# Kernel tuning notes

Hardware: AMD Instinct MI355X
Metric: run time of the kernel (lower is better)

Reference implementation:

```python
import jax, jax.numpy as jnp
import numpy as np

EPS = 1e-5
B, T, D = 4, 2048, 512
H, DK, DV = 4, 64, 128  # num_heads, head_qk_dim, head_v_dim
LR = 32                 # proj_low_rank_dim


def ln(x, g, b):
    m = jnp.mean(x, -1, keepdims=True)
    v = jnp.var(x, -1, keepdims=True)
    return (x - m) * jax.lax.rsqrt(v + EPS) * g + b


def shift(x):  # token shift: zero-pad one step in time
    return jnp.pad(x, ((0, 0), (1, 0), (0, 0)))[:, :-1]


def setup_inputs() -> dict:
    key = jax.random.key(0)
    ks = iter(jax.random.split(key, 40))
    rn = lambda shape, s=0.02: jax.random.normal(next(ks), shape, jnp.float32) * s
    return dict(
        x=jax.random.normal(next(ks), (B, T, D), jnp.float32),
        ln0_g=jnp.ones((D,), jnp.float32), ln0_b=jnp.zeros((D,), jnp.float32),
        ln1_g=jnp.ones((D,), jnp.float32), ln1_b=jnp.zeros((D,), jnp.float32),
        ln2_g=jnp.ones((D,), jnp.float32), ln2_b=jnp.zeros((D,), jnp.float32),
        xp_mu=jax.random.uniform(next(ks), (D,), jnp.float32),
        xp_w1=rn((5 * LR, D)),
        xp_w2=rn((D, 5 * LR)),
        x_bias=rn((5, D)),
        r_w=rn((H * DK, D)),
        w_A=rn((64, D)), w_B=rn((H * DK, 64)), w_b=rn((H * DK,)),
        k_w=rn((H * DK, D)),
        v_w=rn((H * DV, D)),
        g_w=rn((H * DV, D)),
        bonus=rn((H, DK)),
        gn_g=jnp.ones((DV,), jnp.float32), gn_b=jnp.zeros((DV,), jnp.float32),
        o_w=rn((D, H * DV)),
        fk_mu=jax.random.uniform(next(ks), (D,), jnp.float32),
        fk_w=rn((1024, D)),
        fr_mu=jax.random.uniform(next(ks), (D,), jnp.float32),
        fr_w=rn((D, D)),
        fv_w=rn((D, 1024)),
    )


def reference(x, ln0_g, ln0_b, ln1_g, ln1_b, ln2_g, ln2_b, xp_mu, xp_w1, xp_w2,
              x_bias, r_w, w_A, w_B, w_b, k_w, v_w, g_w, bonus, gn_g, gn_b,
              o_w, fk_mu, fk_w, fr_mu, fr_w, fv_w):
    # --- block pre-norm (layer_idx==0) and attn norm ---
    residual = ln(x, ln0_g, ln0_b)
    h = ln(residual, ln1_g, ln1_b)

    # --- RWKV6 time mixing ---
    delta = shift(h) - h
    xx = jnp.tanh(((h + delta * xp_mu) @ xp_w1.T).reshape(B, T, 5, LR))
    mods = jnp.einsum('btnr,hnr->btnh', xx, xp_w2.reshape(D, 5, LR)) + x_bias
    mr, mw, mk, mv, mg = (mods[:, :, i] for i in range(5))

    r = ((h + delta * mr) @ r_w.T).reshape(B, T, H, DK)
    wl = jnp.tanh((h + delta * mw) @ w_A.T) @ w_B.T + w_b  # LoRA decay proj
    dec = jnp.exp(-jnp.exp(wl)).reshape(B, T, H, DK)       # per-channel decay in (0,1)
    k = ((h + delta * mk) @ k_w.T).reshape(B, T, H, DK)
    v = ((h + delta * mv) @ v_w.T).reshape(B, T, H, DV)
    g = (h + delta * mg) @ g_w.T

    def step(S, inp):
        r_t, k_t, v_t, d_t = inp                           # (B,H,DK),(B,H,DK),(B,H,DV),(B,H,DK)
        kv = k_t[..., :, None] * v_t[..., None, :]          # (B,H,DK,DV)
        o_t = jnp.einsum('bhk,bhkv->bhv', r_t, S + bonus[None, :, :, None] * kv)
        S = d_t[..., None] * S + kv
        return S, o_t

    tf = lambda a: jnp.moveaxis(a, 1, 0)  # time-major for scan
    S0 = jnp.zeros((B, H, DK, DV), x.dtype)
    _, o = jax.lax.scan(step, S0, (tf(r), tf(k), tf(v), tf(dec)))
    o = jnp.moveaxis(o, 0, 1)  # (B,T,H,DV)

    # fused per-head LayerNorm + swish gate, then output proj
    gg = g.reshape(B, T, H, DV)
    o = ln(o, gn_g, gn_b) * (gg * jax.nn.sigmoid(gg))
    a = o.reshape(B, T, H * DV) @ o_w.T

    # --- channel mixing FFN with residual ---
    z = a + residual
    h2 = ln(z, ln2_g, ln2_b)
    d2 = shift(h2) - h2
    kk = jnp.square(jax.nn.relu((h2 + d2 * fk_mu) @ fk_w.T))
    rr = jax.nn.sigmoid((h2 + d2 * fr_mu) @ fr_w.T)
    return z + rr * (kk @ fv_w.T)
```

## Files before the change

### kernel.cpp

```cpp
#include <hip/hip_runtime.h>
#include <math.h>

constexpr int Bq = 4, Tq = 2048, Dq = 512, Hq = 4, DKq = 64, DVq = 128, LRq = 32;
constexpr int Mq = Bq * Tq;
constexpr float EPSq = 1e-5f;
constexpr int CL2 = 32, NC2 = Tq / CL2, BH2 = Bq * Hq;

typedef unsigned short u16;
typedef __attribute__((ext_vector_type(8))) short short8v;
typedef __attribute__((ext_vector_type(4))) float f32x4;

__device__ __forceinline__ u16 f2b(float f) {
    unsigned u = __float_as_uint(f);
    u += 0x7fffu + ((u >> 16) & 1);
    return (u16)(u >> 16);
}

__device__ __forceinline__ void gl_lds16(const void* g, void* l) {
    __builtin_amdgcn_global_load_lds(
        (const __attribute__((address_space(1))) unsigned int*)g,
        (__attribute__((address_space(3))) unsigned int*)l, 16, 0, 0);
}

__global__ __launch_bounds__(256)
void k_ln01(const float* __restrict__ x,
            const float* __restrict__ g0, const float* __restrict__ b0,
            const float* __restrict__ g1, const float* __restrict__ b1,
            float* __restrict__ Rout, float* __restrict__ Hout) {
    __shared__ float red[8];
    int row = blockIdx.x, tid = threadIdx.x;
    const float* xr = x + (size_t)row * Dq;
    float v0 = xr[tid], v1 = xr[tid + 256];

    float s = v0 + v1, q = v0 * v0 + v1 * v1;
#pragma unroll
    for (int o = 32; o; o >>= 1) { s += __shfl_down(s, o); q += __shfl_down(q, o); }
    if ((tid & 63) == 0) { red[tid >> 6] = s; red[4 + (tid >> 6)] = q; }
    __syncthreads();
    s = red[0] + red[1] + red[2] + red[3];
    q = red[4] + red[5] + red[6] + red[7];
    float mean = s * (1.f / Dq);
    float inv = rsqrtf(q * (1.f / Dq) - mean * mean + EPSq);
    float r0 = (v0 - mean) * inv * g0[tid] + b0[tid];
    float r1 = (v1 - mean) * inv * g0[tid + 256] + b0[tid + 256];
    Rout[(size_t)row * Dq + tid] = r0;
    Rout[(size_t)row * Dq + tid + 256] = r1;

    s = r0 + r1; q = r0 * r0 + r1 * r1;
#pragma unroll
    for (int o = 32; o; o >>= 1) { s += __shfl_down(s, o); q += __shfl_down(q, o); }
    __syncthreads();
    if ((tid & 63) == 0) { red[tid >> 6] = s; red[4 + (tid >> 6)] = q; }
    __syncthreads();
    s = red[0] + red[1] + red[2] + red[3];
    q = red[4] + red[5] + red[6] + red[7];
    mean = s * (1.f / Dq);
    inv = rsqrtf(q * (1.f / Dq) - mean * mean + EPSq);
    Hout[(size_t)row * Dq + tid] = (r0 - mean) * inv * g1[tid] + b1[tid];
    Hout[(size_t)row * Dq + tid + 256] = (r1 - mean) * inv * g1[tid + 256] + b1[tid + 256];
}

__global__ __launch_bounds__(256)
void k_mix1(const float* __restrict__ h, const float* __restrict__ mu,
            u16* __restrict__ out) {
    int row = blockIdx.x, t = row % Tq;
    const float* hr = h + (size_t)row * Dq;
#pragma unroll
    for (int it = 0; it < 2; it++) {
        int d = threadIdx.x + it * 256;
        float hv = hr[d];
        float pv = t ? hr[d - Dq] : 0.f;
        out[(size_t)row * Dq + d] = f2b(hv + (pv - hv) * mu[d]);
    }
}

__global__ __launch_bounds__(256)
void k_ln2mix(const float* __restrict__ Z,
              const float* __restrict__ g2, const float* __restrict__ b2,
              const float* __restrict__ muK, const float* __restrict__ muR,
              u16* __restrict__ outK, u16* __restrict__ outR) {
    __shared__ float red[16];
    int row = blockIdx.x, t = row % Tq, tid = threadIdx.x;
    const float* zr = Z + (size_t)row * Dq;
    float c0 = zr[tid], c1 = zr[tid + 256];
    float p0 = 0.f, p1 = 0.f;
    if (t) { p0 = zr[tid - Dq]; p1 = zr[tid + 256 - Dq]; }
    float sc = c0 + c1, qc = c0 * c0 + c1 * c1;
    float sp = p0 + p1, qp = p0 * p0 + p1 * p1;
#pragma unroll
    for (int o = 32; o; o >>= 1) {
        sc += __shfl_down(sc, o); qc += __shfl_down(qc, o);
        sp += __shfl_down(sp, o); qp += __shfl_down(qp, o);
    }
    if ((tid & 63) == 0) {
        int w = tid >> 6;
        red[w] = sc; red[4 + w] = qc; red[8 + w] = sp; red[12 + w] = qp;
    }
    __syncthreads();
    sc = red[0] + red[1] + red[2] + red[3];
    qc = red[4] + red[5] + red[6] + red[7];
    sp = red[8] + red[9] + red[10] + red[11];
    qp = red[12] + red[13] + red[14] + red[15];
    float mc = sc * (1.f / Dq), ic = rsqrtf(qc * (1.f / Dq) - mc * mc + EPSq);
    float mp = sp * (1.f / Dq), ip = rsqrtf(qp * (1.f / Dq) - mp * mp + EPSq);
#pragma unroll
    for (int it = 0; it < 2; it++) {
        int d = tid + it * 256;
        float cv = it ? c1 : c0, pv = it ? p1 : p0;
        float hc = (cv - mc) * ic * g2[d] + b2[d];
        float hp = t ? ((pv - mp) * ip * g2[d] + b2[d]) : 0.f;
        float dl = hp - hc;
        outK[(size_t)row * Dq + d] = f2b(hc + dl * muK[d]);
        outR[(size_t)row * Dq + d] = f2b(hc + dl * muR[d]);
    }
}

struct WConv {
    const float* src[11];
    u16* dst[11];
    int n[11];
    int npad[11];
};
__global__ __launch_bounds__(256)
void k_wconv(WConv wc) {
    int w = blockIdx.y;
    const float* s = wc.src[w];
    u16* d = wc.dst[w];
    int n = wc.n[w], np = wc.npad[w];
    for (int i = blockIdx.x * 256 + threadIdx.x; i < np; i += gridDim.x * 256)
        d[i] = (i < n) ? f2b(s[i]) : (u16)0;
}

enum MEpi { ME_NONE, ME_TANH_F32, ME_TANH_B16, ME_DECAY, ME_RESID,
            ME_RELUSQ_B16, ME_SIGMOID, ME_GATED };

template <int EPI>
__global__ __launch_bounds__(256)
void k_mgemm(const u16* __restrict__ A, int lda,
             const u16* __restrict__ W, int ldw,
             void* __restrict__ Cout, int ldc,
             int N, int K,
             const float* __restrict__ bias,
             const float* __restrict__ P1,
             const float* __restrict__ P2) {
    __shared__ __align__(16) char smem[32768];
    char* sA = smem;
    char* sB = smem + 16384;
    const int m0 = blockIdx.x * 128, n0 = blockIdx.y * 128;
    const int tid = threadIdx.x, lane = tid & 63, wid = tid >> 6;
    const int wm = wid >> 1, wn = wid & 1;

    f32x4 acc[4][4] = {};

    const int rl = lane >> 3;
    const int ccs = (lane & 7) ^ rl;
    const u16* ga = A + (size_t)(m0 + wid * 32 + rl) * lda + ccs * 8;
    const u16* gb = W + (size_t)(n0 + wid * 32 + rl) * ldw + ccs * 8;
    char* la = sA + (wid * 32) * 128;
    char* lb = sB + (wid * 32) * 128;

    const int nkt = K >> 6;
    for (int kt = 0; kt < nkt; ++kt) {
        const int k0 = kt << 6;
#pragma unroll
        for (int i = 0; i < 4; ++i) {
            gl_lds16(ga + (size_t)(i * 8) * lda + k0, la + i * 8 * 128);
            gl_lds16(gb + (size_t)(i * 8) * ldw + k0, lb + i * 8 * 128);
        }
        asm volatile("s_waitcnt vmcnt(0)" ::: "memory");
        __syncthreads();
#pragma unroll
        for (int ks = 0; ks < 2; ++ks) {
            short8v af[4], bfr[4];
            const int cc = ks * 4 + (lane >> 4);
#pragma unroll
            for (int i = 0; i < 4; ++i) {
                const int mr = wm * 64 + i * 16 + (lane & 15);
                af[i] = *(const short8v*)(sA + mr * 128 + ((cc ^ (mr & 7)) << 4));
                const int nr = wn * 64 + i * 16 + (lane & 15);
                bfr[i] = *(const short8v*)(sB + nr * 128 + ((cc ^ (nr & 7)) << 4));
            }
#pragma unroll
            for (int i = 0; i < 4; ++i)
#pragma unroll
                for (int j = 0; j < 4; ++j)
                    acc[i][j] = __builtin_amdgcn_mfma_f32_16x16x32_bf16(
                        af[i], bfr[j], acc[i][j], 0, 0, 0);
        }
        __syncthreads();
    }

    float* Cf = (float*)Cout;
    u16* Cb = (u16*)Cout;
#pragma unroll
    for (int i = 0; i < 4; ++i) {
        const int row = m0 + wm * 64 + i * 16 + (lane >> 4) * 4;
#pragma unroll
        for (int j = 0; j < 4; ++j) {
            const int col = n0 + wn * 64 + j * 16 + (lane & 15);
            if (col < N) {
#pragma unroll
                for (int r = 0; r < 4; ++r) {
                    const float v = acc[i][j][r];
                    const size_t idx = (size_t)(row + r) * ldc + col;
                    if constexpr (EPI == ME_NONE)        Cf[idx] = v;
                    else if constexpr (EPI == ME_TANH_F32) Cf[idx] = tanhf(v);
                    else if constexpr (EPI == ME_TANH_B16) Cb[idx] = f2b(tanhf(v));
                    else if constexpr (EPI == ME_DECAY)  Cf[idx] = expf(-expf(v + bias[col]));
                    else if constexpr (EPI == ME_RESID)  Cf[idx] = v + P1[idx];
                    else if constexpr (EPI == ME_RELUSQ_B16) {
                        float t = fmaxf(v, 0.f); Cb[idx] = f2b(t * t);
                    }
                    else if constexpr (EPI == ME_SIGMOID) Cf[idx] = 1.f / (1.f + __expf(-v));
                    else                                  Cf[idx] = P1[idx] + P2[idx] * v;
                }
            }
        }
    }
}

struct GemmDesc {
    const u16* A; const u16* W; void* C;
    int lda, ldw, ldc, N, K, epi;
};
struct MultiDesc {
    GemmDesc g[5];
    int gid[16];
    int ntile[16];
};

__global__ __launch_bounds__(256)
void k_mgemm_multi(MultiDesc md) {
    __shared__ __align__(16) char smem[32768];
    char* sA = smem;
    char* sB = smem + 16384;
    const GemmDesc d = md.g[md.gid[blockIdx.y]];
    const int m0 = blockIdx.x * 128, n0 = md.ntile[blockIdx.y] * 128;
    const int tid = threadIdx.x, lane = tid & 63, wid = tid >> 6;
    const int wm = wid >> 1, wn = wid & 1;

    f32x4 acc[4][4] = {};

    const int rl = lane >> 3;
    const int ccs = (lane & 7) ^ rl;
    const u16* ga = d.A + (size_t)(m0 + wid * 32 + rl) * d.lda + ccs * 8;
    const u16* gb = d.W + (size_t)(n0 + wid * 32 + rl) * d.ldw + ccs * 8;
    char* la = sA + (wid * 32) * 128;
    char* lb = sB + (wid * 32) * 128;

    const int nkt = d.K >> 6;
    for (int kt = 0; kt < nkt; ++kt) {
        const int k0 = kt << 6;
#pragma unroll
        for (int i = 0; i < 4; ++i) {
            gl_lds16(ga + (size_t)(i * 8) * d.lda + k0, la + i * 8 * 128);
            gl_lds16(gb + (size_t)(i * 8) * d.ldw + k0, lb + i * 8 * 128);
        }
        asm volatile("s_waitcnt vmcnt(0)" ::: "memory");
        __syncthreads();
#pragma unroll
        for (int ks = 0; ks < 2; ++ks) {
            short8v af[4], bfr[4];
            const int cc = ks * 4 + (lane >> 4);
#pragma unroll
            for (int i = 0; i < 4; ++i) {
                const int mr = wm * 64 + i * 16 + (lane & 15);
                af[i] = *(const short8v*)(sA + mr * 128 + ((cc ^ (mr & 7)) << 4));
                const int nr = wn * 64 + i * 16 + (lane & 15);
                bfr[i] = *(const short8v*)(sB + nr * 128 + ((cc ^ (nr & 7)) << 4));
            }
#pragma unroll
            for (int i = 0; i < 4; ++i)
#pragma unroll
                for (int j = 0; j < 4; ++j)
                    acc[i][j] = __builtin_amdgcn_mfma_f32_16x16x32_bf16(
                        af[i], bfr[j], acc[i][j], 0, 0, 0);
        }
        __syncthreads();
    }

    float* Cf = (float*)d.C;
    u16* Cb = (u16*)d.C;
#pragma unroll
    for (int i = 0; i < 4; ++i) {
        const int row = m0 + wm * 64 + i * 16 + (lane >> 4) * 4;
#pragma unroll
        for (int j = 0; j < 4; ++j) {
            const int col = n0 + wn * 64 + j * 16 + (lane & 15);
            if (col < d.N) {
#pragma unroll
                for (int r = 0; r < 4; ++r) {
                    const float v = acc[i][j][r];
                    const size_t idx = (size_t)(row + r) * d.ldc + col;
                    if (d.epi == 0)      Cf[idx] = v;
                    else if (d.epi == 1) Cb[idx] = f2b(tanhf(v));
                    else if (d.epi == 2) { float t = fmaxf(v, 0.f); Cb[idx] = f2b(t * t); }
                    else                 Cf[idx] = 1.f / (1.f + __expf(-v));
                }
            }
        }
    }
}

__global__ __launch_bounds__(256)
void k_gemm_mix5(const float* __restrict__ XX, const float* __restrict__ w2,
                 const float* __restrict__ xb, const float* __restrict__ Hb,
                 u16* __restrict__ AMX) {
    constexpr int BM = 64, BK = 16, K = LRq, LDX = 5 * LRq;
    __shared__ __align__(16) float sA[BK][BM + 4];
    __shared__ __align__(16) float sB[BK][BM + 4];
    int g = blockIdx.z;
    const float* A = XX + g * LRq;
    const float* W = w2 + g * LRq;
    const float* bias = xb + g * Dq;
    u16* C = AMX + (size_t)g * Mq * Dq;
    int m0 = blockIdx.x * BM, n0 = blockIdx.y * BM;
    int tid = threadIdx.x;
    int tx = tid & 15, ty = tid >> 4;
    int lr = tid >> 2, lc = (tid & 3) * 4;
    float acc[4][4] = {};

    for (int k0 = 0; k0 < K; k0 += BK) {
        float4 av = *(const float4*)(A + (size_t)(m0 + lr) * LDX + k0 + lc);
        float4 bv = *(const float4*)(W + (size_t)(n0 + lr) * LDX + k0 + lc);
        sA[lc + 0][lr] = av.x; sA[lc + 1][lr] = av.y;
        sA[lc + 2][lr] = av.z; sA[lc + 3][lr] = av.w;
        sB[lc + 0][lr] = bv.x; sB[lc + 1][lr] = bv.y;
        sB[lc + 2][lr] = bv.z; sB[lc + 3][lr] = bv.w;
        __syncthreads();
#pragma unroll
        for (int kk = 0; kk < BK; kk++) {
            float4 a4 = *(const float4*)&sA[kk][ty * 4];
            float4 b4 = *(const float4*)&sB[kk][tx * 4];
            acc[0][0] += a4.x * b4.x; acc[0][1] += a4.x * b4.y;
            acc[0][2] += a4.x * b4.z; acc[0][3] += a4.x * b4.w;
            acc[1][0] += a4.y * b4.x; acc[1][1] += a4.y * b4.y;
            acc[1][2] += a4.y * b4.z; acc[1][3] += a4.y * b4.w;
            acc[2][0] += a4.z * b4.x; acc[2][1] += a4.z * b4.y;
            acc[2][2] += a4.z * b4.z; acc[2][3] += a4.z * b4.w;
            acc[3][0] += a4.w * b4.x; acc[3][1] += a4.w * b4.y;
            acc[3][2] += a4.w * b4.z; acc[3][3] += a4.w * b4.w;
        }
        __syncthreads();
    }

#pragma unroll
    for (int i = 0; i < 4; i++) {
        int row = m0 + ty * 4 + i;
        int t = row % Tq;
#pragma unroll
        for (int j = 0; j < 4; j++) {
            int col = n0 + tx * 4 + j;
            size_t idx = (size_t)row * Dq + col;
            float val = acc[i][j] + bias[col];
            float hv = Hb[idx];
            float pv = t ? Hb[idx - Dq] : 0.f;
            C[idx] = f2b(hv + (pv - hv) * val);
        }
    }
}

__global__ __launch_bounds__(256)
void k_prep_m(const float* __restrict__ Rp, const float* __restrict__ Kp,
              const float* __restrict__ Dp, const float* __restrict__ Vp,
              const float* __restrict__ bonus,
              float* __restrict__ RQd, float* __restrict__ KQg,
              float* __restrict__ DIAG, float* __restrict__ PC,
              float* __restrict__ MC) {
    int c = blockIdx.x, bh = blockIdx.y;
    int b = bh >> 2, h = bh & 3;
    __shared__ float Rl[CL2][68], Kl[CL2][68], Dl[CL2][68];
    __shared__ float Vl[CL2][128];
    __shared__ float Pl[64];
    int tid = threadIdx.x;
#pragma unroll
    for (int i = 0; i < 8; i++) {
        int idx = i * 256 + tid;
        int t = idx >> 6, k = idx & 63;
        size_t g = ((size_t)(b * Tq + c * CL2 + t) * Hq + h) * DKq + k;
        Rl[t][k] = Rp[g]; Kl[t][k] = Kp[g]; Dl[t][k] = Dp[g];
    }
#pragma unroll
    for (int i = 0; i < 16; i++) {
        int idx = i * 256 + tid;
        int t = idx >> 7, v = idx & 127;
        Vl[t][v] = Vp[((size_t)(b * Tq + c * CL2 + t) * Hq + h) * DVq + v];
    }
    __syncthreads();
    {
        int t = tid >> 3, kg = tid & 7;
        float p = 0.f;
#pragma unroll
        for (int i = 0; i < 8; i++) {
            int k = kg * 8 + i;
            p += Rl[t][k] * Kl[t][k] * bonus[h * DKq + k];
        }
        p += __shfl_down(p, 4, 8);
        p += __shfl_down(p, 2, 8);
        p += __shfl_down(p, 1, 8);
        if (kg == 0) DIAG[(size_t)bh * Tq + c * CL2 + t] = p;
    }
    __syncthreads();
    if (tid < 64) {
        int k = tid;
        float p = 1.f;
        for (int t = 0; t < CL2; t++) {
            float d = Dl[t][k];
            Rl[t][k] *= p;
            p *= d;
            Kl[t][k] /= p;
        }
        Pl[k] = p;
    }
    __syncthreads();
#pragma unroll
    for (int i = 0; i < 8; i++) {
        int idx = i * 256 + tid;
        int t = idx >> 6, k = idx & 63;
        size_t g = ((size_t)bh * Tq + c * CL2 + t) * DKq + k;
        RQd[g] = Rl[t][k];
        KQg[g] = Kl[t][k];
    }
    if (tid < 64) PC[(size_t)(bh * NC2 + c) * DKq + tid] = Pl[tid];
    {
        int tk = tid >> 5, tv = tid & 31;
        float acc[8][4] = {};
        for (int t = 0; t < CL2; t++) {
            float4 ka = *(const float4*)&Kl[t][tk * 8];
            float4 kb = *(const float4*)&Kl[t][tk * 8 + 4];
            float4 v4 = *(const float4*)&Vl[t][tv * 4];
            float kv[8] = {ka.x, ka.y, ka.z, ka.w, kb.x, kb.y, kb.z, kb.w};
#pragma unroll
            for (int i = 0; i < 8; i++) {
                acc[i][0] = fmaf(kv[i], v4.x, acc[i][0]);
                acc[i][1] = fmaf(kv[i], v4.y, acc[i][1]);
                acc[i][2] = fmaf(kv[i], v4.z, acc[i][2]);
                acc[i][3] = fmaf(kv[i], v4.w, acc[i][3]);
            }
        }
#pragma unroll
        for (int i = 0; i < 8; i++) {
            int k = tk * 8 + i;
            float P = Pl[k];
            *(float4*)&MC[((size_t)(bh * NC2 + c) * DKq + k) * DVq + tv * 4] =
                make_float4(acc[i][0] * P, acc[i][1] * P, acc[i][2] * P, acc[i][3] * P);
        }
    }
}

__global__ __launch_bounds__(256)
void k_combine2(float* __restrict__ S0MC, const float* __restrict__ PC) {
    int idx = blockIdx.x * 256 + threadIdx.x;
    int v = idx & 127;
    int k = (idx >> 7) & 63;
    int bh = idx >> 13;
    float s = 0.f;
    for (int c = 0; c < NC2; c++) {
        size_t p = (size_t)(bh * NC2 + c) * DKq + k;
        size_t m = p * DVq + v;
        float mc = S0MC[m];
        S0MC[m] = s;
        s = fmaf(PC[p], s, mc);
    }
}

__global__ __launch_bounds__(256)
void k_scan_o(const float* __restrict__ RQd, const float* __restrict__ KQg,
              const float* __restrict__ Vp, const float* __restrict__ S0,
              const float* __restrict__ DIAG, const float* __restrict__ Gp,
              const float* __restrict__ gng, const float* __restrict__ gnb,
              u16* __restrict__ OB) {
    int c = blockIdx.x, bh = blockIdx.y;
    int b = bh >> 2, h = bh & 3;
    __shared__ float RQl[CL2][68];
    __shared__ float KQt[DKq][36];
    __shared__ float Vl[CL2][128];
    __shared__ float S0l[DKq][128];
    __shared__ float Al[CL2][33];
    int tid = threadIdx.x;
#pragma unroll
    for (int i = 0; i < 8; i++) {
        int idx = i * 256 + tid;
        int t = idx >> 6, k = idx & 63;
        size_t g = ((size_t)bh * Tq + c * CL2 + t) * DKq + k;
        RQl[t][k] = RQd[g];
        KQt[k][t] = KQg[g];
    }
#pragma unroll
    for (int i = 0; i < 16; i++) {
        int idx = i * 256 + tid;
        int t = idx >> 7, v = idx & 127;
        Vl[t][v] = Vp[((size_t)(b * Tq + c * CL2 + t) * Hq + h) * DVq + v];
    }
#pragma unroll
    for (int i = 0; i < 32; i++) {
        int idx = i * 256 + tid;
        int k = idx >> 7, v = idx & 127;
        S0l[k][v] = S0[((size_t)(bh * NC2 + c) * DKq + k) * DVq + v];
    }
    __syncthreads();
    {
        int t = tid >> 3, sq = tid & 7;
        float a[4] = {};
        for (int k = 0; k < DKq; k++) {
            float rq = RQl[t][k];
            float4 k4 = *(const float4*)&KQt[k][sq * 4];
            a[0] = fmaf(rq, k4.x, a[0]);
            a[1] = fmaf(rq, k4.y, a[1]);
            a[2] = fmaf(rq, k4.z, a[2]);
            a[3] = fmaf(rq, k4.w, a[3]);
        }
        float diag = DIAG[(size_t)bh * Tq + c * CL2 + t];
#pragma unroll
        for (int j = 0; j < 4; j++) {
            int s = sq * 4 + j;
            Al[t][s] = (s < t) ? a[j] : (s == t ? diag : 0.f);
        }
    }
    __syncthreads();
    {
        int t = tid >> 3, vg = tid & 7;
        float o[16] = {};
        for (int s = 0; s <= t; s++) {
            float a = Al[t][s];
#pragma unroll
            for (int q = 0; q < 4; q++) {
                float4 v4 = *(const float4*)&Vl[s][vg * 4 + q * 32];
                o[q * 4 + 0] = fmaf(a, v4.x, o[q * 4 + 0]);
                o[q * 4 + 1] = fmaf(a, v4.y, o[q * 4 + 1]);
                o[q * 4 + 2] = fmaf(a, v4.z, o[q * 4 + 2]);
                o[q * 4 + 3] = fmaf(a, v4.w, o[q * 4 + 3]);
            }
        }
        for (int k = 0; k < DKq; k++) {
            float rq = RQl[t][k];
#pragma unroll
            for (int q = 0; q < 4; q++) {
                float4 s4 = *(const float4*)&S0l[k][vg * 4 + q * 32];
                o[q * 4 + 0] = fmaf(rq, s4.x, o[q * 4 + 0]);
                o[q * 4 + 1] = fmaf(rq, s4.y, o[q * 4 + 1]);
                o[q * 4 + 2] = fmaf(rq, s4.z, o[q * 4 + 2]);
                o[q * 4 + 3] = fmaf(rq, s4.w, o[q * 4 + 3]);
            }
        }
        float s = 0.f, q = 0.f;
#pragma unroll
        for (int i = 0; i < 16; i++) { s += o[i]; q += o[i] * o[i]; }
#pragma unroll
        for (int off = 4; off; off >>= 1) { s += __shfl_xor(s, off); q += __shfl_xor(q, off); }
        float mean = s * (1.f / DVq);
        float inv = rsqrtf(q * (1.f / DVq) - mean * mean + EPSq);
        size_t gb = ((size_t)(b * Tq + c * CL2 + t) * Hq + h) * DVq;
#pragma unroll
        for (int qd = 0; qd < 4; qd++) {
            int v0i = vg * 4 + qd * 32;
            float4 g4 = *(const float4*)&Gp[gb + v0i];
            ushort4 ob;
            float lnv, gv;
            gv = g4.x; lnv = (o[qd * 4 + 0] - mean) * inv * gng[v0i + 0] + gnb[v0i + 0];
            ob.x = f2b(lnv * (gv / (1.f + __expf(-gv))));
            gv = g4.y; lnv = (o[qd * 4 + 1] - mean) * inv * gng[v0i + 1] + gnb[v0i + 1];
            ob.y = f2b(lnv * (gv / (1.f + __expf(-gv))));
            gv = g4.z; lnv = (o[qd * 4 + 2] - mean) * inv * gng[v0i + 2] + gnb[v0i + 2];
            ob.z = f2b(lnv * (gv / (1.f + __expf(-gv))));
            gv = g4.w; lnv = (o[qd * 4 + 3] - mean) * inv * gng[v0i + 3] + gnb[v0i + 3];
            ob.w = f2b(lnv * (gv / (1.f + __expf(-gv))));
            *(ushort4*)&OB[gb + v0i] = ob;
        }
    }
}

extern "C" void kernel_launch(void* const* d_in, const int* in_sizes, int n_in,
                              void* d_out, int out_size, void* d_ws, size_t ws_size,
                              hipStream_t stream) {
    const float* x     = (const float*)d_in[0];
    const float* ln0_g = (const float*)d_in[1];
    const float* ln0_b = (const float*)d_in[2];
    const float* ln1_g = (const float*)d_in[3];
    const float* ln1_b = (const float*)d_in[4];
    const float* ln2_g = (const float*)d_in[5];
    const float* ln2_b = (const float*)d_in[6];
    const float* xp_mu = (const float*)d_in[7];
    const float* xp_w1 = (const float*)d_in[8];
    const float* xp_w2 = (const float*)d_in[9];
    const float* x_bias= (const float*)d_in[10];
    const float* r_w   = (const float*)d_in[11];
    const float* w_A   = (const float*)d_in[12];
    const float* w_B   = (const float*)d_in[13];
    const float* w_b   = (const float*)d_in[14];
    const float* k_w   = (const float*)d_in[15];
    const float* v_w   = (const float*)d_in[16];
    const float* g_w   = (const float*)d_in[17];
    const float* bonus = (const float*)d_in[18];
    const float* gn_g  = (const float*)d_in[19];
    const float* gn_b  = (const float*)d_in[20];
    const float* o_w   = (const float*)d_in[21];
    const float* fk_mu = (const float*)d_in[22];
    const float* fk_w  = (const float*)d_in[23];
    const float* fr_mu = (const float*)d_in[24];
    const float* fr_w  = (const float*)d_in[25];
    const float* fv_w  = (const float*)d_in[26];
    float* out = (float*)d_out;
    (void)in_sizes; (void)n_in; (void)out_size; (void)ws_size;

    const size_t MD = (size_t)Mq * Dq;
    float* ws = (float*)d_ws;
    size_t off = 0;
    auto af32 = [&](size_t n) { float* p = ws + off; off += n; return p; };

    float* R    = af32(MD);
    float* Hb   = af32(MD);
    float* XX   = af32((size_t)Mq * 160);
    float* Rproj= af32((size_t)Mq * 256);
    float* DEC  = af32((size_t)Mq * 256);
    float* KB   = af32((size_t)Mq * 256);
    float* VB   = af32(MD);
    float* GB   = af32(MD);
    float* PC   = af32((size_t)BH2 * NC2 * DKq);
    float* S0MC = af32((size_t)BH2 * NC2 * DKq * DVq);
    float* DIAG = af32((size_t)BH2 * Tq);

    u16* us = (u16*)(ws + off);
    size_t uo = 0;
    auto au16 = [&](size_t n) { u16* p = us + uo; uo += n; return p; };
    u16* MX0b = au16(MD);
    u16* AMXb = au16(5 * MD);
    u16* TAb  = au16((size_t)Mq * 64);
    u16* OBb  = au16(MD);
    u16* wb_xp1 = au16(256 * 512);
    u16* wb_r   = au16(256 * 512);
    u16* wb_wA  = au16(128 * 512);
    u16* wb_wB  = au16(256 * 64);
    u16* wb_k   = au16(256 * 512);
    u16* wb_v   = au16(512 * 512);
    u16* wb_g   = au16(512 * 512);
    u16* wb_o   = au16(512 * 512);
    u16* wb_fk  = au16(1024 * 512);
    u16* wb_fr  = au16(512 * 512);
    u16* wb_fv  = au16(512 * 1024);

    float* RQd = (float*)MX0b;
    float* KQg = (float*)(AMXb + 4 * MD);
    float* Z   = GB;
    float* RRb = VB;
    u16* MXKb = AMXb;
    u16* MXRb = AMXb + MD;
    u16* KKb  = AMXb + 2 * MD;

    WConv wc;
    const float* wsrc[11] = {xp_w1, r_w, w_A, w_B, k_w, v_w, g_w, o_w, fk_w, fr_w, fv_w};
    u16* wdst[11] = {wb_xp1, wb_r, wb_wA, wb_wB, wb_k, wb_v, wb_g, wb_o, wb_fk, wb_fr, wb_fv};
    int wn_[11]  = {160*512, 256*512, 64*512, 256*64, 256*512, 512*512, 512*512,
                    512*512, 1024*512, 512*512, 512*1024};
    int wnp[11]  = {256*512, 256*512, 128*512, 256*64, 256*512, 512*512, 512*512,
                    512*512, 1024*512, 512*512, 512*1024};
    for (int i = 0; i < 11; i++) { wc.src[i] = wsrc[i]; wc.dst[i] = wdst[i];
                                   wc.n[i] = wn_[i]; wc.npad[i] = wnp[i]; }
    k_wconv<<<dim3(64, 11), 256, 0, stream>>>(wc);

    k_ln01<<<Mq, 256, 0, stream>>>(x, ln0_g, ln0_b, ln1_g, ln1_b, R, Hb);

    k_mix1<<<Mq, 256, 0, stream>>>(Hb, xp_mu, MX0b);
    k_mgemm<ME_TANH_F32><<<dim3(64, 2), 256, 0, stream>>>(
        MX0b, 512, wb_xp1, 512, XX, 160, 160, 512, nullptr, nullptr, nullptr);

    k_gemm_mix5<<<dim3(128, 8, 5), 256, 0, stream>>>(XX, xp_w2, x_bias, Hb, AMXb);

    {
        MultiDesc md;
        md.g[0] = {AMXb + 0 * MD, wb_r,  (void*)Rproj, 512, 512, 256, 256, 512, 0};
        md.g[1] = {AMXb + 1 * MD, wb_wA, (void*)TAb,   512, 512,  64,  64, 512, 1};
        md.g[2] = {AMXb + 2 * MD, wb_k,  (void*)KB,    512, 512, 256, 256, 512, 0};
        md.g[3] = {AMXb + 3 * MD, wb_v,  (void*)VB,    512, 512, 512, 512, 512, 0};
        md.g[4] = {AMXb + 4 * MD, wb_g,  (void*)GB,    512, 512, 512, 512, 512, 0};
        int gid[16]   = {0,0, 1, 2,2, 3,3,3,3, 4,4,4,4, 0,0,0};
        int ntile[16] = {0,1, 0, 0,1, 0,1,2,3, 0,1,2,3, 0,0,0};
        for (int i = 0; i < 16; i++) { md.gid[i] = gid[i]; md.ntile[i] = ntile[i]; }
        k_mgemm_multi<<<dim3(64, 13), 256, 0, stream>>>(md);
    }
    k_mgemm<ME_DECAY><<<dim3(64, 2), 256, 0, stream>>>(
        TAb, 64, wb_wB, 64, DEC, 256, 256, 64, w_b, nullptr, nullptr);

    k_prep_m<<<dim3(NC2, BH2), 256, 0, stream>>>(Rproj, KB, DEC, VB, bonus,
                                                 RQd, KQg, DIAG, PC, S0MC);
    k_combine2<<<(BH2 * DKq * DVq) / 256, 256, 0, stream>>>(S0MC, PC);
    k_scan_o<<<dim3(NC2, BH2), 256, 0, stream>>>(RQd, KQg, VB, S0MC, DIAG,
                                                 GB, gn_g, gn_b, OBb);

    k_mgemm<ME_RESID><<<dim3(64, 4), 256, 0, stream>>>(
        OBb, 512, wb_o, 512, Z, 512, 512, 512, nullptr, R, nullptr);

    k_ln2mix<<<Mq, 256, 0, stream>>>(Z, ln2_g, ln2_b, fk_mu, fr_mu, MXKb, MXRb);
    {
        MultiDesc md;
        md.g[0] = {MXKb, wb_fk, (void*)KKb, 512, 512, 1024, 1024, 512, 2};
        md.g[1] = {MXRb, wb_fr, (void*)RRb, 512, 512,  512,  512, 512, 3};
        int gid[16]   = {0,0,0,0,0,0,0,0, 1,1,1,1, 0,0,0,0};
        int ntile[16] = {0,1,2,3,4,5,6,7, 0,1,2,3, 0,0,0,0};
        for (int i = 0; i < 16; i++) { md.gid[i] = gid[i]; md.ntile[i] = ntile[i]; }
        k_mgemm_multi<<<dim3(64, 12), 256, 0, stream>>>(md);
    }
    k_mgemm<ME_GATED><<<dim3(64, 4), 256, 0, stream>>>(
        KKb, 1024, wb_fv, 1024, out, 512, 512, 1024, nullptr, Z, RRb);
}
```

Before: 432.6 us.

## Double-buffer LDS tiles in MFMA GEMM kernels to overlap loads with compute

Both GEMM kernels now use two 32KB LDS buffers and issue the global-to-LDS loads for the next K tile before computing on the current one. This hides global load latency behind the MFMA work. Wave priority is raised around the MFMA section with s_setprio. The cost is doubled LDS per block (64KB), which may lower occupancy. It also relies on raw s_barrier plus vmcnt waits for correctness instead of __syncthreads.

After: 408.8 us. 1.06x faster.

```diff
diff --git a/kernel.cpp b/kernel.cpp
--- a/kernel.cpp
+++ b/kernel.cpp
@@ -143,9 +143,7 @@
              const float* __restrict__ bias,
              const float* __restrict__ P1,
              const float* __restrict__ P2) {
-    __shared__ __align__(16) char smem[32768];
-    char* sA = smem;
-    char* sB = smem + 16384;
+    __shared__ __align__(16) char smem[65536];
     const int m0 = blockIdx.x * 128, n0 = blockIdx.y * 128;
     const int tid = threadIdx.x, lane = tid & 63, wid = tid >> 6;
     const int wm = wid >> 1, wn = wid & 1;
@@ -156,19 +154,30 @@
     const int ccs = (lane & 7) ^ rl;
     const u16* ga = A + (size_t)(m0 + wid * 32 + rl) * lda + ccs * 8;
     const u16* gb = W + (size_t)(n0 + wid * 32 + rl) * ldw + ccs * 8;
-    char* la = sA + (wid * 32) * 128;
-    char* lb = sB + (wid * 32) * 128;
-
-    const int nkt = K >> 6;
-    for (int kt = 0; kt < nkt; ++kt) {
+    const int lofs = (wid * 32) * 128;
+
+    auto STAGE = [&](int buf, int kt) {
+        char* la = smem + buf * 32768 + lofs;
+        char* lb = smem + buf * 32768 + 16384 + lofs;
         const int k0 = kt << 6;
 #pragma unroll
         for (int i = 0; i < 4; ++i) {
             gl_lds16(ga + (size_t)(i * 8) * lda + k0, la + i * 8 * 128);
             gl_lds16(gb + (size_t)(i * 8) * ldw + k0, lb + i * 8 * 128);
         }
-        asm volatile("s_waitcnt vmcnt(0)" ::: "memory");
-        __syncthreads();
+    };
+
+    const int nkt = K >> 6;
+    STAGE(0, 0);
+    asm volatile("s_waitcnt vmcnt(0)" ::: "memory");
+    __builtin_amdgcn_s_barrier();
+
+    int cur = 0;
+    for (int kt = 0; kt < nkt; ++kt) {
+        if (kt + 1 < nkt) STAGE(cur ^ 1, kt + 1);
+        const char* sA = smem + cur * 32768;
+        const char* sB = sA + 16384;
+        __builtin_amdgcn_s_setprio(1);
 #pragma unroll
         for (int ks = 0; ks < 2; ++ks) {
             short8v af[4], bfr[4];
@@ -187,7 +196,10 @@
                     acc[i][j] = __builtin_amdgcn_mfma_f32_16x16x32_bf16(
                         af[i], bfr[j], acc[i][j], 0, 0, 0);
         }
-        __syncthreads();
+        __builtin_amdgcn_s_setprio(0);
+        asm volatile("s_waitcnt vmcnt(0)" ::: "memory");
+        __builtin_amdgcn_s_barrier();
+        cur ^= 1;
     }
 
     float* Cf = (float*)Cout;
@@ -231,9 +243,7 @@
 
 __global__ __launch_bounds__(256)
 void k_mgemm_multi(MultiDesc md) {
-    __shared__ __align__(16) char smem[32768];
-    char* sA = smem;
-    char* sB = smem + 16384;
+    __shared__ __align__(16) char smem[65536];
     const GemmDesc d = md.g[md.gid[blockIdx.y]];
     const int m0 = blockIdx.x * 128, n0 = md.ntile[blockIdx.y] * 128;
     const int tid = threadIdx.x, lane = tid & 63, wid = tid >> 6;
@@ -245,19 +255,30 @@
     const int ccs = (lane & 7) ^ rl;
     const u16* ga = d.A + (size_t)(m0 + wid * 32 + rl) * d.lda + ccs * 8;
     const u16* gb = d.W + (size_t)(n0 + wid * 32 + rl) * d.ldw + ccs * 8;
-    char* la = sA + (wid * 32) * 128;
-    char* lb = sB + (wid * 32) * 128;
-
-    const int nkt = d.K >> 6;
-    for (int kt = 0; kt < nkt; ++kt) {
+    const int lofs = (wid * 32) * 128;
+
+    auto STAGE = [&](int buf, int kt) {
+        char* la = smem + buf * 32768 + lofs;
+        char* lb = smem + buf * 32768 + 16384 + lofs;
         const int k0 = kt << 6;
 #pragma unroll
         for (int i = 0; i < 4; ++i) {
             gl_lds16(ga + (size_t)(i * 8) * d.lda + k0, la + i * 8 * 128);
             gl_lds16(gb + (size_t)(i * 8) * d.ldw + k0, lb + i * 8 * 128);
         }
-        asm volatile("s_waitcnt vmcnt(0)" ::: "memory");
-        __syncthreads();
+    };
+
+    const int nkt = d.K >> 6;
+    STAGE(0, 0);
+    asm volatile("s_waitcnt vmcnt(0)" ::: "memory");
+    __builtin_amdgcn_s_barrier();
+
+    int cur = 0;
+    for (int kt = 0; kt < nkt; ++kt) {
+        if (kt + 1 < nkt) STAGE(cur ^ 1, kt + 1);
+        const char* sA = smem + cur * 32768;
+        const char* sB = sA + 16384;
+        __builtin_amdgcn_s_setprio(1);
 #pragma unroll
         for (int ks = 0; ks < 2; ++ks) {
             short8v af[4], bfr[4];
@@ -276,7 +297,10 @@
                     acc[i][j] = __builtin_amdgcn_mfma_f32_16x16x32_bf16(
                         af[i], bfr[j], acc[i][j], 0, 0, 0);
         }
-        __syncthreads();
+        __builtin_amdgcn_s_setprio(0);
+        asm volatile("s_waitcnt vmcnt(0)" ::: "memory");
+        __builtin_amdgcn_s_barrier();
+        cur ^= 1;
     }
 
     float* Cf = (float*)d.C;
```
